# Kernel tuning notes

Measured on AMD Instinct MI355X. Metric: run time of the kernel, lower is better.

## Reference

```python
import jax, jax.numpy as jnp
import numpy as np

N_HEADS = 8
D_EMBED = 512
D_HEAD = D_EMBED // N_HEADS


def setup_inputs() -> dict:
    key = jax.random.key(0)
    ks = jax.random.split(key, 5)
    x = jax.random.normal(ks[0], (1, 4096, D_EMBED), dtype=jnp.float32)
    # in_proj: Linear(d, 3d); out_proj: Linear(d, d). Stored as [in, out] for x @ W.
    scale_in = 1.0 / np.sqrt(D_EMBED)
    W_in = jax.random.uniform(ks[1], (D_EMBED, 3 * D_EMBED), jnp.float32, -scale_in, scale_in)
    b_in = jax.random.uniform(ks[2], (3 * D_EMBED,), jnp.float32, -scale_in, scale_in)
    W_out = jax.random.uniform(ks[3], (D_EMBED, D_EMBED), jnp.float32, -scale_in, scale_in)
    b_out = jax.random.uniform(ks[4], (D_EMBED,), jnp.float32, -scale_in, scale_in)
    return {"x": x, "W_in": W_in, "b_in": b_in, "W_out": W_out, "b_out": b_out,
            "causal_mask": 1}


def reference(x, W_in, b_in, W_out, b_out, causal_mask):
    B, S, D = x.shape
    qkv = x @ W_in + b_in                      # [B, S, 3D]
    q, k, v = jnp.split(qkv, 3, axis=-1)
    # [B, S, D] -> [B, H, S, d_head]
    def split_heads(t):
        return t.reshape(B, S, N_HEADS, D_HEAD).transpose(0, 2, 1, 3)
    q, k, v = split_heads(q), split_heads(k), split_heads(v)
    weight = jnp.einsum("bhqd,bhkd->bhqk", q, k)  # [B, H, S, S]
    if causal_mask:
        mask = jnp.triu(jnp.ones((S, S), dtype=bool), k=1)
        weight = jnp.where(mask, -jnp.inf, weight)
    weight = weight / jnp.sqrt(jnp.float32(D_HEAD)).astype(weight.dtype)
    weight = jax.nn.softmax(weight, axis=-1)
    out = jnp.einsum("bhqk,bhkd->bhqd", weight, v)  # [B, H, S, d_head]
    out = out.transpose(0, 2, 1, 3).reshape(B, S, D)
    return out @ W_out + b_out
```

## Files before the change

kernel.cpp:

```cpp
#include <hip/hip_runtime.h>
#include <math.h>

#define SEQ 4096
#define DM 512
#define NH 8
#define DH 64
#define TQK (3 * DM)
#define QSCALE 0.18033688011112042f

typedef __attribute__((ext_vector_type(8))) short bf16x8;
typedef __attribute__((ext_vector_type(4))) float floatx4;
typedef unsigned short ushort_t;

__device__ __forceinline__ floatx4 mfma16(bf16x8 a, bf16x8 b, floatx4 c) {
    return __builtin_amdgcn_mfma_f32_16x16x32_bf16(a, b, c, 0, 0, 0);
}
__device__ __forceinline__ float ex2(float x) { return __builtin_amdgcn_exp2f(x); }

__device__ __forceinline__ unsigned int pk2(float a, float b) {
    unsigned int ua = __float_as_uint(a); ua = (ua + 0x7FFFu + ((ua >> 16) & 1u)) >> 16;
    unsigned int ub = __float_as_uint(b); ub = (ub + 0x7FFFu + ((ub >> 16) & 1u)) >> 16;
    return ua | (ub << 16);
}
__device__ __forceinline__ unsigned short f2bf(float x) {
    unsigned int u = __float_as_uint(x);
    return (unsigned short)((u + 0x7FFFu + ((u >> 16) & 1u)) >> 16);
}
__device__ __forceinline__ float bflo(unsigned int u) { return __uint_as_float(u << 16); }
__device__ __forceinline__ float bfhi(unsigned int u) { return __uint_as_float(u & 0xFFFF0000u); }

__device__ __forceinline__ void gload_lds16(const void* g, void* l) {
    __builtin_amdgcn_global_load_lds(
        (const __attribute__((address_space(1))) unsigned int*)g,
        (__attribute__((address_space(3))) unsigned int*)l, 16, 0, 0);
}

#define DPPMAX(x, ctrl) \
    (x) = fmaxf((x), __int_as_float(__builtin_amdgcn_update_dpp(0, __float_as_int(x), (ctrl), 0xF, 0xF, true)))
__device__ __forceinline__ float row_max16(float x) {
    DPPMAX(x, 0xB1);
    DPPMAX(x, 0x4E);
    DPPMAX(x, 0x141);
    DPPMAX(x, 0x140);
    return x;
}

__global__ __launch_bounds__(256) void prep(const float* __restrict__ x,
                                            const float* __restrict__ W_in,
                                            const float* __restrict__ W_out,
                                            ushort_t* __restrict__ xb,
                                            ushort_t* __restrict__ wti,
                                            ushort_t* __restrict__ wto) {
    __shared__ float T[64][65];
    const int bid = blockIdx.x, tid = threadIdx.x;
    if (bid < 1024) {
        const int i = bid * 256 + tid;
        const float4* p = (const float4*)x + (size_t)i * 2;
        float4 f0 = p[0], f1 = p[1];
        ((uint4*)xb)[i] = make_uint4(pk2(f0.x, f0.y), pk2(f0.z, f0.w),
                                     pk2(f1.x, f1.y), pk2(f1.z, f1.w));
        return;
    }
    const float* W; ushort_t* WT; int N, K, n0, k0; bool qscale;
    if (bid < 1216) { int id = bid - 1024; W = W_in;  WT = wti; N = TQK; K = DM;
                      n0 = (id % 24) * 64; k0 = (id / 24) * 64; qscale = true; }
    else            { int id = bid - 1216; W = W_out; WT = wto; N = DM;  K = DM;
                      n0 = (id % 8) * 64;  k0 = (id / 8) * 64;  qscale = false; }
    {
        const int r = tid >> 2, g = tid & 3;
        const float* src = W + (size_t)(k0 + r) * N + n0 + g * 16;
#pragma unroll
        for (int i = 0; i < 4; i++) {
            float4 f = ((const float4*)src)[i];
            T[g * 16 + i * 4 + 0][r] = f.x;
            T[g * 16 + i * 4 + 1][r] = f.y;
            T[g * 16 + i * 4 + 2][r] = f.z;
            T[g * 16 + i * 4 + 3][r] = f.w;
        }
    }
    __syncthreads();
    const int nr = tid >> 2, g2 = tid & 3;
    const float sc = (qscale && (n0 + nr < DM)) ? QSCALE : 1.0f;
    unsigned int pk[8];
#pragma unroll
    for (int j = 0; j < 8; j++)
        pk[j] = pk2(T[nr][g2 * 16 + 2 * j] * sc, T[nr][g2 * 16 + 2 * j + 1] * sc);
    ushort_t* dst = WT + (size_t)(n0 + nr) * K + k0 + g2 * 16;
    ((uint4*)dst)[0] = make_uint4(pk[0], pk[1], pk[2], pk[3]);
    ((uint4*)dst)[1] = make_uint4(pk[4], pk[5], pk[6], pk[7]);
}

template <bool OUT_BF16>
__global__ __launch_bounds__(256) void gemm128(const ushort_t* __restrict__ A,
                                               const ushort_t* __restrict__ BT,
                                               const float* __restrict__ bias,
                                               void* __restrict__ Cv,
                                               ushort_t* __restrict__ vt_out,
                                               int N, int K, int scale_q) {
    __shared__ __align__(16) ushort_t As[2][128 * 64];
    __shared__ __align__(16) ushort_t Bs[2][128 * 64];
    const int tid  = threadIdx.x;
    const int lane = tid & 63;
    const int w    = tid >> 6;
    const int quad = lane >> 4;
    const int ln   = lane & 15;
    const int row0 = blockIdx.y * 128;
    const int col0 = blockIdx.x * 128;
    const int wm = w >> 1, wn = w & 1;

    const int srow = lane >> 3;
    const int js   = (lane & 7) ^ srow;

    floatx4 acc[4][4];
#pragma unroll
    for (int i = 0; i < 4; i++)
#pragma unroll
        for (int j = 0; j < 4; j++) acc[i][j] = (floatx4){0.f, 0.f, 0.f, 0.f};

    const int nsteps = K >> 6;
#pragma unroll
    for (int i = 0; i < 4; i++) {
        const int c = w * 4 + i;
        gload_lds16(A  + (size_t)(row0 + c * 8 + srow) * K + js * 8, &As[0][c * 512]);
        gload_lds16(BT + (size_t)(col0 + c * 8 + srow) * K + js * 8, &Bs[0][c * 512]);
    }

    for (int kt = 0; kt < nsteps; kt++) {
        const int cur = kt & 1;
        __syncthreads();
        if (kt + 1 < nsteps) {
            const int k0n = (kt + 1) << 6;
#pragma unroll
            for (int i = 0; i < 4; i++) {
                const int c = w * 4 + i;
                gload_lds16(A  + (size_t)(row0 + c * 8 + srow) * K + k0n + js * 8, &As[cur ^ 1][c * 512]);
                gload_lds16(BT + (size_t)(col0 + c * 8 + srow) * K + k0n + js * 8, &Bs[cur ^ 1][c * 512]);
            }
        }
#pragma unroll
        for (int s = 0; s < 2; s++) {
            bf16x8 af[4], bfr[4];
#pragma unroll
            for (int i = 0; i < 4; i++) {
                const int lm = wm * 64 + i * 16 + ln;
                af[i] = *(const bf16x8*)&As[cur][lm * 64 + ((s * 4 + quad) ^ (ln & 7)) * 8];
                const int lnn = wn * 64 + i * 16 + ln;
                bfr[i] = *(const bf16x8*)&Bs[cur][lnn * 64 + ((s * 4 + quad) ^ (ln & 7)) * 8];
            }
#pragma unroll
            for (int i = 0; i < 4; i++)
#pragma unroll
                for (int j = 0; j < 4; j++)
                    acc[i][j] = mfma16(af[i], bfr[j], acc[i][j]);
        }
    }

    if (vt_out && col0 >= 2 * DM) {
#pragma unroll
        for (int j = 0; j < 4; j++) {
            const int n = col0 + wn * 64 + j * 16 + ln;
            const float bv = bias[n];
#pragma unroll
            for (int i = 0; i < 4; i++) {
                const int mb = row0 + wm * 64 + i * 16 + quad * 4;
                uint2 pkd;
                pkd.x = pk2(acc[i][j][0] + bv, acc[i][j][1] + bv);
                pkd.y = pk2(acc[i][j][2] + bv, acc[i][j][3] + bv);
                *(uint2*)&vt_out[(size_t)(n - 2 * DM) * SEQ + mb] = pkd;
            }
        }
        return;
    }

#pragma unroll
    for (int j = 0; j < 4; j++) {
        const int n = col0 + wn * 64 + j * 16 + ln;
        const float bv = bias[n] * ((scale_q && n < DM) ? QSCALE : 1.0f);
#pragma unroll
        for (int i = 0; i < 4; i++) {
            const int mb = row0 + wm * 64 + i * 16 + quad * 4;
#pragma unroll
            for (int r = 0; r < 4; r++) {
                const float v = acc[i][j][r] + bv;
                if (OUT_BF16) ((ushort_t*)Cv)[(size_t)(mb + r) * N + n] = f2bf(v);
                else          ((float*)Cv)[(size_t)(mb + r) * N + n] = v;
            }
        }
    }
}

__global__ __launch_bounds__(256) void attn_split(const ushort_t* __restrict__ qkv_b,
                                                  const ushort_t* __restrict__ vt,
                                                  ushort_t* __restrict__ po,
                                                  float2* __restrict__ pml) {
    __shared__ __align__(16) ushort_t Ks[2][64 * 64];
    __shared__ __align__(16) ushort_t Vs[2][64 * 64];
    __shared__ __align__(16) ushort_t Ps[64 * 72];

    const int tid  = threadIdx.x;
    const int lane = tid & 63;
    const int w    = tid >> 6;
    const int quad = lane >> 4;
    const int ln   = lane & 15;
    const int h    = blockIdx.y;

    const int e = 287 - (int)blockIdx.x;
    int k = 1;
    while (e >= 4 * k * (k + 1)) k++;
    const int off = e - 4 * k * (k - 1);
    const int qt  = 8 * (k - 1) + off / k;
    const int c   = off % k;
    const int nc  = k;
    const int T   = qt + 1;
    const int jt0 = (c * T) / nc;
    const int jt1 = ((c + 1) * T) / nc;
    const int q0  = qt * 64;

    const ushort_t* qrow = qkv_b + (size_t)(q0 + w * 16 + ln) * TQK + h * DH;
    const bf16x8 a0 = *(const bf16x8*)(qrow + quad * 8);
    const bf16x8 a1 = *(const bf16x8*)(qrow + quad * 8 + 32);

    const short oneb = (short)0x3F80;
    const bf16x8 vone = {oneb, oneb, oneb, oneb, oneb, oneb, oneb, oneb};

    float m_q = -INFINITY;
    floatx4 o[4], ol;
#pragma unroll
    for (int t = 0; t < 4; t++) o[t] = (floatx4){0.f, 0.f, 0.f, 0.f};
    ol = (floatx4){0.f, 0.f, 0.f, 0.f};

    const int srow = lane >> 3;
    const int js   = (lane & 7) ^ srow;

    {
        const int k0 = jt0 * 64;
#pragma unroll
        for (int i = 0; i < 2; i++) {
            const int cg = w * 2 + i;
            gload_lds16(qkv_b + (size_t)(k0 + cg * 8 + srow) * TQK + DM + h * DH + js * 8,
                        &Ks[0][cg * 512]);
            gload_lds16(vt + (size_t)(h * DH + cg * 8 + srow) * SEQ + k0 + js * 8,
                        &Vs[0][cg * 512]);
        }
    }

    for (int jt = jt0; jt < jt1; ++jt) {
        const int cur = (jt - jt0) & 1;
        __syncthreads();
        if (jt + 1 < jt1) {
            const int k0n = (jt + 1) * 64;
#pragma unroll
            for (int i = 0; i < 2; i++) {
                const int cg = w * 2 + i;
                gload_lds16(qkv_b + (size_t)(k0n + cg * 8 + srow) * TQK + DM + h * DH + js * 8,
                            &Ks[cur ^ 1][cg * 512]);
                gload_lds16(vt + (size_t)(h * DH + cg * 8 + srow) * SEQ + k0n + js * 8,
                            &Vs[cur ^ 1][cg * 512]);
            }
        }

        floatx4 sa[4];
#pragma unroll
        for (int t = 0; t < 4; t++) {
            const int n = t * 16 + ln;
            const bf16x8 b0 = *(const bf16x8*)&Ks[cur][n * 64 + ((quad) ^ (ln & 7)) * 8];
            const bf16x8 b1 = *(const bf16x8*)&Ks[cur][n * 64 + ((4 + quad) ^ (ln & 7)) * 8];
            floatx4 acc = {0.f, 0.f, 0.f, 0.f};
            acc = mfma16(a0, b0, acc);
            acc = mfma16(a1, b1, acc);
            sa[t] = acc;
        }

        if (jt == qt) {
#pragma unroll
            for (int t = 0; t < 4; t++) {
                const int cg2 = t * 16 + ln;
#pragma unroll
                for (int r = 0; r < 4; r++) {
                    const int rg = w * 16 + quad * 4 + r;
                    if (cg2 > rg) sa[t][r] = -INFINITY;
                }
            }
        }

        float mx = sa[0][0];
#pragma unroll
        for (int t = 0; t < 4; t++)
#pragma unroll
            for (int r = 0; r < 4; r++) mx = fmaxf(mx, sa[t][r]);
        mx = row_max16(mx);
        const float mn = fmaxf(m_q, mx);
        const float alpha = ex2(m_q - mn);
        m_q = mn;
#pragma unroll
        for (int t = 0; t < 4; t++)
#pragma unroll
            for (int r = 0; r < 4; r++) {
                const float p = ex2(sa[t][r] - mn);
                Ps[(w * 16 + quad * 4 + r) * 72 + t * 16 + ln] =
                    (ushort_t)(__float_as_uint(p) >> 16);
            }
        if (alpha < 1.0f) {
#pragma unroll
            for (int t = 0; t < 4; t++)
#pragma unroll
                for (int r = 0; r < 4; r++) o[t][r] *= alpha;
#pragma unroll
            for (int r = 0; r < 4; r++) ol[r] *= alpha;
        }

        __builtin_amdgcn_wave_barrier();

        const bf16x8 p0 = *(const bf16x8*)&Ps[(w * 16 + ln) * 72 + quad * 8];
        const bf16x8 p1 = *(const bf16x8*)&Ps[(w * 16 + ln) * 72 + quad * 8 + 32];
#pragma unroll
        for (int t = 0; t < 4; t++) {
            const int d = t * 16 + ln;
            const bf16x8 v0 = *(const bf16x8*)&Vs[cur][d * 64 + ((quad) ^ (ln & 7)) * 8];
            const bf16x8 v1 = *(const bf16x8*)&Vs[cur][d * 64 + ((4 + quad) ^ (ln & 7)) * 8];
            o[t] = mfma16(p0, v0, o[t]);
            o[t] = mfma16(p1, v1, o[t]);
        }
        ol = mfma16(p0, vone, ol);
        ol = mfma16(p1, vone, ol);
    }

    const size_t pbase  = ((size_t)h * 288 + e) * 4096;
    const size_t mlbase = ((size_t)h * 288 + e) * 64;
#pragma unroll
    for (int t = 0; t < 4; t++)
#pragma unroll
        for (int r = 0; r < 4; r++)
            po[pbase + (size_t)(w * 16 + quad * 4 + r) * 64 + t * 16 + ln] = f2bf(o[t][r]);
    if (ln == 0) {
#pragma unroll
        for (int r = 0; r < 4; r++)
            pml[mlbase + w * 16 + quad * 4 + r] = make_float2(m_q, ol[r]);
    }
}

__global__ __launch_bounds__(256) void attn_combine(const ushort_t* __restrict__ po,
                                                    const float2* __restrict__ pml,
                                                    ushort_t* __restrict__ aob) {
    const int qt = blockIdx.x, h = blockIdx.y;
    const int k = (qt >> 3) + 1;
    const int sbase = 4 * k * (k - 1) + (qt & 7) * k;
    const int nc = k;
    const int row = threadIdx.x >> 2, g = threadIdx.x & 3;

    float2 ml[8];
    float M = -INFINITY;
    for (int cidx = 0; cidx < nc; cidx++) {
        ml[cidx] = pml[((size_t)h * 288 + sbase + cidx) * 64 + row];
        M = fmaxf(M, ml[cidx].x);
    }
    float L = 0.f;
    float acc[16];
#pragma unroll
    for (int j = 0; j < 16; j++) acc[j] = 0.f;

    for (int cidx = 0; cidx < nc; cidx++) {
        const float wgt = ex2(ml[cidx].x - M);
        L += wgt * ml[cidx].y;
        const ushort_t* p = po + ((size_t)h * 288 + sbase + cidx) * 4096 + (size_t)row * 64 + g * 16;
        uint4 u0 = ((const uint4*)p)[0];
        uint4 u1 = ((const uint4*)p)[1];
        const unsigned int uu[8] = {u0.x, u0.y, u0.z, u0.w, u1.x, u1.y, u1.z, u1.w};
#pragma unroll
        for (int j = 0; j < 8; j++) {
            acc[2 * j]     += wgt * bflo(uu[j]);
            acc[2 * j + 1] += wgt * bfhi(uu[j]);
        }
    }
    const float inv = 1.0f / L;
    unsigned int pk[8];
#pragma unroll
    for (int j = 0; j < 8; j++)
        pk[j] = pk2(acc[2 * j] * inv, acc[2 * j + 1] * inv);
    ushort_t* dst = aob + (size_t)(qt * 64 + row) * DM + h * DH + g * 16;
    ((uint4*)dst)[0] = make_uint4(pk[0], pk[1], pk[2], pk[3]);
    ((uint4*)dst)[1] = make_uint4(pk[4], pk[5], pk[6], pk[7]);
}

extern "C" void kernel_launch(void* const* d_in, const int* in_sizes, int n_in,
                              void* d_out, int out_size, void* d_ws, size_t ws_size,
                              hipStream_t stream) {
    const float* x     = (const float*)d_in[0];
    const float* W_in  = (const float*)d_in[1];
    const float* b_in  = (const float*)d_in[2];
    const float* W_out = (const float*)d_in[3];
    const float* b_out = (const float*)d_in[4];
    float* out = (float*)d_out;

    char* ws = (char*)d_ws;
    ushort_t* xb    = (ushort_t*)ws;
    ushort_t* wti   = (ushort_t*)(ws + (4u  << 20));
    ushort_t* wto   = (ushort_t*)(ws + (6u  << 20));
    ushort_t* qkv_b = (ushort_t*)(ws + (7u  << 20));
    ushort_t* vtb   = (ushort_t*)(ws + (19u << 20));
    ushort_t* aob   = (ushort_t*)(ws + (23u << 20));
    ushort_t* po    = (ushort_t*)(ws + (27u << 20));
    float2*   pml   = (float2*)  (ws + (46u << 20));

    prep<<<1280, 256, 0, stream>>>(x, W_in, W_out, xb, wti, wto);

    gemm128<true><<<dim3(TQK / 128, SEQ / 128), 256, 0, stream>>>(
        xb, wti, b_in, qkv_b, vtb, TQK, DM, 1);

    attn_split<<<dim3(288, NH), 256, 0, stream>>>(qkv_b, vtb, po, pml);

    attn_combine<<<dim3(SEQ / 64, NH), 256, 0, stream>>>(po, pml, aob);

    gemm128<false><<<dim3(DM / 128, SEQ / 128), 256, 0, stream>>>(
        aob, wto, b_out, out, nullptr, DM, DM, 0);
}
```

Before: 173.7 us.

## Fuse split-KV combine into output GEMM and widen attention tiles to 128 queries

The attention split kernel now handles 128 query rows per block with 8 waves, halving the number of split work items and sharing each K/V tile load across twice as many queries. Causal masking becomes per-wave, with a clamp on the running max so fully masked rows stay finite. The separate combine kernel is removed: the output projection GEMM merges the partial results for each head directly into its LDS A tile, which drops the intermediate attention-output buffer and one launch. In exchange, each output-GEMM block redoes the combine for its rows once per column tile, and its global loads sit in the K-loop.

Result: no change. 173.4 us (-0.2%).

```diff
diff --git a/kernel.cpp b/kernel.cpp
--- a/kernel.cpp
+++ b/kernel.cpp
@@ -90,13 +90,11 @@
     ((uint4*)dst)[1] = make_uint4(pk[4], pk[5], pk[6], pk[7]);
 }
 
-template <bool OUT_BF16>
-__global__ __launch_bounds__(256) void gemm128(const ushort_t* __restrict__ A,
+__global__ __launch_bounds__(256) void gemm_in(const ushort_t* __restrict__ A,
                                                const ushort_t* __restrict__ BT,
                                                const float* __restrict__ bias,
-                                               void* __restrict__ Cv,
-                                               ushort_t* __restrict__ vt_out,
-                                               int N, int K, int scale_q) {
+                                               ushort_t* __restrict__ Cv,
+                                               ushort_t* __restrict__ vt_out) {
     __shared__ __align__(16) ushort_t As[2][128 * 64];
     __shared__ __align__(16) ushort_t Bs[2][128 * 64];
     const int tid  = threadIdx.x;
@@ -107,9 +105,9 @@
     const int row0 = blockIdx.y * 128;
     const int col0 = blockIdx.x * 128;
     const int wm = w >> 1, wn = w & 1;
-
     const int srow = lane >> 3;
     const int js   = (lane & 7) ^ srow;
+    const int K = DM, N = TQK;
 
     floatx4 acc[4][4];
 #pragma unroll
@@ -117,7 +115,6 @@
 #pragma unroll
         for (int j = 0; j < 4; j++) acc[i][j] = (floatx4){0.f, 0.f, 0.f, 0.f};
 
-    const int nsteps = K >> 6;
 #pragma unroll
     for (int i = 0; i < 4; i++) {
         const int c = w * 4 + i;
@@ -125,10 +122,10 @@
         gload_lds16(BT + (size_t)(col0 + c * 8 + srow) * K + js * 8, &Bs[0][c * 512]);
     }
 
-    for (int kt = 0; kt < nsteps; kt++) {
+    for (int kt = 0; kt < 8; kt++) {
         const int cur = kt & 1;
         __syncthreads();
-        if (kt + 1 < nsteps) {
+        if (kt < 7) {
             const int k0n = (kt + 1) << 6;
 #pragma unroll
             for (int i = 0; i < 4; i++) {
@@ -155,7 +152,7 @@
         }
     }
 
-    if (vt_out && col0 >= 2 * DM) {
+    if (col0 >= 2 * DM) {
 #pragma unroll
         for (int j = 0; j < 4; j++) {
             const int n = col0 + wn * 64 + j * 16 + ln;
@@ -175,27 +172,24 @@
 #pragma unroll
     for (int j = 0; j < 4; j++) {
         const int n = col0 + wn * 64 + j * 16 + ln;
-        const float bv = bias[n] * ((scale_q && n < DM) ? QSCALE : 1.0f);
+        const float bv = bias[n] * ((n < DM) ? QSCALE : 1.0f);
 #pragma unroll
         for (int i = 0; i < 4; i++) {
             const int mb = row0 + wm * 64 + i * 16 + quad * 4;
 #pragma unroll
-            for (int r = 0; r < 4; r++) {
-                const float v = acc[i][j][r] + bv;
-                if (OUT_BF16) ((ushort_t*)Cv)[(size_t)(mb + r) * N + n] = f2bf(v);
-                else          ((float*)Cv)[(size_t)(mb + r) * N + n] = v;
-            }
-        }
-    }
-}
-
-__global__ __launch_bounds__(256) void attn_split(const ushort_t* __restrict__ qkv_b,
+            for (int r = 0; r < 4; r++)
+                Cv[(size_t)(mb + r) * N + n] = f2bf(acc[i][j][r] + bv);
+        }
+    }
+}
+
+__global__ __launch_bounds__(512) void attn_split(const ushort_t* __restrict__ qkv_b,
                                                   const ushort_t* __restrict__ vt,
                                                   ushort_t* __restrict__ po,
                                                   float2* __restrict__ pml) {
     __shared__ __align__(16) ushort_t Ks[2][64 * 64];
     __shared__ __align__(16) ushort_t Vs[2][64 * 64];
-    __shared__ __align__(16) ushort_t Ps[64 * 72];
+    __shared__ __align__(16) ushort_t Ps[128 * 72];
 
     const int tid  = threadIdx.x;
     const int lane = tid & 63;
@@ -204,17 +198,17 @@
     const int ln   = lane & 15;
     const int h    = blockIdx.y;
 
-    const int e = 287 - (int)blockIdx.x;
-    int k = 1;
-    while (e >= 4 * k * (k + 1)) k++;
-    const int off = e - 4 * k * (k - 1);
-    const int qt  = 8 * (k - 1) + off / k;
-    const int c   = off % k;
-    const int nc  = k;
-    const int T   = qt + 1;
+    const int e = 143 - (int)blockIdx.x;
+    int g = 0;
+    while (e >= 2 * (g + 1) * (g + 2)) g++;
+    const int off = e - 2 * g * (g + 1);
+    const int nc  = g + 1;
+    const int qt  = 4 * g + off / nc;
+    const int c   = off % nc;
+    const int T   = 2 * qt + 2;
     const int jt0 = (c * T) / nc;
     const int jt1 = ((c + 1) * T) / nc;
-    const int q0  = qt * 64;
+    const int q0  = qt * 128;
 
     const ushort_t* qrow = qkv_b + (size_t)(q0 + w * 16 + ln) * TQK + h * DH;
     const bf16x8 a0 = *(const bf16x8*)(qrow + quad * 8);
@@ -234,29 +228,22 @@
 
     {
         const int k0 = jt0 * 64;
-#pragma unroll
-        for (int i = 0; i < 2; i++) {
-            const int cg = w * 2 + i;
-            gload_lds16(qkv_b + (size_t)(k0 + cg * 8 + srow) * TQK + DM + h * DH + js * 8,
-                        &Ks[0][cg * 512]);
-            gload_lds16(vt + (size_t)(h * DH + cg * 8 + srow) * SEQ + k0 + js * 8,
-                        &Vs[0][cg * 512]);
-        }
+        gload_lds16(qkv_b + (size_t)(k0 + w * 8 + srow) * TQK + DM + h * DH + js * 8,
+                    &Ks[0][w * 512]);
+        gload_lds16(vt + (size_t)(h * DH + w * 8 + srow) * SEQ + k0 + js * 8,
+                    &Vs[0][w * 512]);
     }
 
     for (int jt = jt0; jt < jt1; ++jt) {
         const int cur = (jt - jt0) & 1;
+        const int k0  = jt * 64;
         __syncthreads();
         if (jt + 1 < jt1) {
             const int k0n = (jt + 1) * 64;
-#pragma unroll
-            for (int i = 0; i < 2; i++) {
-                const int cg = w * 2 + i;
-                gload_lds16(qkv_b + (size_t)(k0n + cg * 8 + srow) * TQK + DM + h * DH + js * 8,
-                            &Ks[cur ^ 1][cg * 512]);
-                gload_lds16(vt + (size_t)(h * DH + cg * 8 + srow) * SEQ + k0n + js * 8,
-                            &Vs[cur ^ 1][cg * 512]);
-            }
+            gload_lds16(qkv_b + (size_t)(k0n + w * 8 + srow) * TQK + DM + h * DH + js * 8,
+                        &Ks[cur ^ 1][w * 512]);
+            gload_lds16(vt + (size_t)(h * DH + w * 8 + srow) * SEQ + k0n + js * 8,
+                        &Vs[cur ^ 1][w * 512]);
         }
 
         floatx4 sa[4];
@@ -271,13 +258,13 @@
             sa[t] = acc;
         }
 
-        if (jt == qt) {
+        if (k0 + 63 > q0 + w * 16) {
 #pragma unroll
             for (int t = 0; t < 4; t++) {
-                const int cg2 = t * 16 + ln;
+                const int cg2 = k0 + t * 16 + ln;
 #pragma unroll
                 for (int r = 0; r < 4; r++) {
-                    const int rg = w * 16 + quad * 4 + r;
+                    const int rg = q0 + w * 16 + quad * 4 + r;
                     if (cg2 > rg) sa[t][r] = -INFINITY;
                 }
             }
@@ -289,7 +276,7 @@
 #pragma unroll
             for (int r = 0; r < 4; r++) mx = fmaxf(mx, sa[t][r]);
         mx = row_max16(mx);
-        const float mn = fmaxf(m_q, mx);
+        const float mn = fmaxf(fmaxf(m_q, mx), -1e30f);
         const float alpha = ex2(m_q - mn);
         m_q = mn;
 #pragma unroll
@@ -325,8 +312,8 @@
         ol = mfma16(p1, vone, ol);
     }
 
-    const size_t pbase  = ((size_t)h * 288 + e) * 4096;
-    const size_t mlbase = ((size_t)h * 288 + e) * 64;
+    const size_t pbase  = ((size_t)h * 144 + e) * (128 * 64);
+    const size_t mlbase = ((size_t)h * 144 + e) * 128;
 #pragma unroll
     for (int t = 0; t < 4; t++)
 #pragma unroll
@@ -339,47 +326,123 @@
     }
 }
 
-__global__ __launch_bounds__(256) void attn_combine(const ushort_t* __restrict__ po,
-                                                    const float2* __restrict__ pml,
-                                                    ushort_t* __restrict__ aob) {
-    const int qt = blockIdx.x, h = blockIdx.y;
-    const int k = (qt >> 3) + 1;
-    const int sbase = 4 * k * (k - 1) + (qt & 7) * k;
-    const int nc = k;
-    const int row = threadIdx.x >> 2, g = threadIdx.x & 3;
-
-    float2 ml[8];
-    float M = -INFINITY;
-    for (int cidx = 0; cidx < nc; cidx++) {
-        ml[cidx] = pml[((size_t)h * 288 + sbase + cidx) * 64 + row];
-        M = fmaxf(M, ml[cidx].x);
-    }
-    float L = 0.f;
-    float acc[16];
-#pragma unroll
-    for (int j = 0; j < 16; j++) acc[j] = 0.f;
-
-    for (int cidx = 0; cidx < nc; cidx++) {
-        const float wgt = ex2(ml[cidx].x - M);
-        L += wgt * ml[cidx].y;
-        const ushort_t* p = po + ((size_t)h * 288 + sbase + cidx) * 4096 + (size_t)row * 64 + g * 16;
-        uint4 u0 = ((const uint4*)p)[0];
-        uint4 u1 = ((const uint4*)p)[1];
-        const unsigned int uu[8] = {u0.x, u0.y, u0.z, u0.w, u1.x, u1.y, u1.z, u1.w};
-#pragma unroll
-        for (int j = 0; j < 8; j++) {
-            acc[2 * j]     += wgt * bflo(uu[j]);
-            acc[2 * j + 1] += wgt * bfhi(uu[j]);
-        }
-    }
-    const float inv = 1.0f / L;
-    unsigned int pk[8];
-#pragma unroll
-    for (int j = 0; j < 8; j++)
-        pk[j] = pk2(acc[2 * j] * inv, acc[2 * j + 1] * inv);
-    ushort_t* dst = aob + (size_t)(qt * 64 + row) * DM + h * DH + g * 16;
-    ((uint4*)dst)[0] = make_uint4(pk[0], pk[1], pk[2], pk[3]);
-    ((uint4*)dst)[1] = make_uint4(pk[4], pk[5], pk[6], pk[7]);
+__global__ __launch_bounds__(512) void gemm_out(const ushort_t* __restrict__ po,
+                                                const float2* __restrict__ pml,
+                                                const ushort_t* __restrict__ BT,
+                                                const float* __restrict__ bias,
+                                                float* __restrict__ out) {
+    __shared__ __align__(16) ushort_t As[2][128 * 72];
+    __shared__ __align__(16) ushort_t Bs[2][128 * 64];
+    const int tid  = threadIdx.x;
+    const int lane = tid & 63;
+    const int w    = tid >> 6;
+    const int quad = lane >> 4;
+    const int ln   = lane & 15;
+    const int row0 = blockIdx.y * 128;
+    const int col0 = blockIdx.x * 128;
+    const int wm = w >> 2, wn = w & 3;
+    const int srow = lane >> 3;
+    const int js   = (lane & 7) ^ srow;
+
+    const int qt = blockIdx.y;
+    const int gq = qt >> 2;
+    const int nc = gq + 1;
+    const int sbase = 2 * gq * (gq + 1) + (qt & 3) * nc;
+
+    const int cr = tid >> 2, cg = tid & 3;
+
+    floatx4 acc[4][2];
+#pragma unroll
+    for (int i = 0; i < 4; i++)
+#pragma unroll
+        for (int j = 0; j < 2; j++) acc[i][j] = (floatx4){0.f, 0.f, 0.f, 0.f};
+
+    auto combine = [&](int head, int buf) {
+        float2 ml[8];
+        float M = -INFINITY;
+        for (int ci = 0; ci < nc; ci++) {
+            ml[ci] = pml[((size_t)head * 144 + sbase + ci) * 128 + cr];
+            M = fmaxf(M, ml[ci].x);
+        }
+        float L = 0.f;
+        float a[16];
+#pragma unroll
+        for (int j = 0; j < 16; j++) a[j] = 0.f;
+        for (int ci = 0; ci < nc; ci++) {
+            const float wgt = ex2(ml[ci].x - M);
+            L += wgt * ml[ci].y;
+            const ushort_t* p = po + ((size_t)head * 144 + sbase + ci) * (128 * 64)
+                                   + (size_t)cr * 64 + cg * 16;
+            uint4 u0 = ((const uint4*)p)[0];
+            uint4 u1 = ((const uint4*)p)[1];
+            const unsigned int uu[8] = {u0.x, u0.y, u0.z, u0.w, u1.x, u1.y, u1.z, u1.w};
+#pragma unroll
+            for (int j = 0; j < 8; j++) {
+                a[2 * j]     += wgt * bflo(uu[j]);
+                a[2 * j + 1] += wgt * bfhi(uu[j]);
+            }
+        }
+        const float inv = 1.0f / L;
+        unsigned int pk[8];
+#pragma unroll
+        for (int j = 0; j < 8; j++)
+            pk[j] = pk2(a[2 * j] * inv, a[2 * j + 1] * inv);
+        uint4* dst = (uint4*)&As[buf][cr * 72 + cg * 16];
+        dst[0] = make_uint4(pk[0], pk[1], pk[2], pk[3]);
+        dst[1] = make_uint4(pk[4], pk[5], pk[6], pk[7]);
+    };
+    auto loadB = [&](int kt, int buf) {
+#pragma unroll
+        for (int i = 0; i < 2; i++) {
+            const int cgrp = w * 2 + i;
+            gload_lds16(BT + (size_t)(col0 + cgrp * 8 + srow) * DM + kt * 64 + js * 8,
+                        &Bs[buf][cgrp * 512]);
+        }
+    };
+
+    loadB(0, 0);
+    combine(0, 0);
+
+    for (int kt = 0; kt < 8; kt++) {
+        const int cur = kt & 1;
+        __syncthreads();
+        if (kt < 7) {
+            loadB(kt + 1, cur ^ 1);
+            combine(kt + 1, cur ^ 1);
+        }
+#pragma unroll
+        for (int s = 0; s < 2; s++) {
+            bf16x8 af[4], bfr[2];
+#pragma unroll
+            for (int i = 0; i < 4; i++) {
+                const int lm = wm * 64 + i * 16 + ln;
+                af[i] = *(const bf16x8*)&As[cur][lm * 72 + (s * 4 + quad) * 8];
+            }
+#pragma unroll
+            for (int j = 0; j < 2; j++) {
+                const int lnn = wn * 32 + j * 16 + ln;
+                bfr[j] = *(const bf16x8*)&Bs[cur][lnn * 64 + ((s * 4 + quad) ^ (ln & 7)) * 8];
+            }
+#pragma unroll
+            for (int i = 0; i < 4; i++)
+#pragma unroll
+                for (int j = 0; j < 2; j++)
+                    acc[i][j] = mfma16(af[i], bfr[j], acc[i][j]);
+        }
+    }
+
+#pragma unroll
+    for (int j = 0; j < 2; j++) {
+        const int n = col0 + wn * 32 + j * 16 + ln;
+        const float bv = bias[n];
+#pragma unroll
+        for (int i = 0; i < 4; i++) {
+            const int mb = row0 + wm * 64 + i * 16 + quad * 4;
+#pragma unroll
+            for (int r = 0; r < 4; r++)
+                out[(size_t)(mb + r) * DM + n] = acc[i][j][r] + bv;
+        }
+    }
 }
 
 extern "C" void kernel_launch(void* const* d_in, const int* in_sizes, int n_in,
@@ -398,19 +461,14 @@
     ushort_t* wto   = (ushort_t*)(ws + (6u  << 20));
     ushort_t* qkv_b = (ushort_t*)(ws + (7u  << 20));
     ushort_t* vtb   = (ushort_t*)(ws + (19u << 20));
-    ushort_t* aob   = (ushort_t*)(ws + (23u << 20));
-    ushort_t* po    = (ushort_t*)(ws + (27u << 20));
-    float2*   pml   = (float2*)  (ws + (46u << 20));
+    ushort_t* po    = (ushort_t*)(ws + (23u << 20));
+    float2*   pml   = (float2*)  (ws + (42u << 20));
 
     prep<<<1280, 256, 0, stream>>>(x, W_in, W_out, xb, wti, wto);
 
-    gemm128<true><<<dim3(TQK / 128, SEQ / 128), 256, 0, stream>>>(
-        xb, wti, b_in, qkv_b, vtb, TQK, DM, 1);
-
-    attn_split<<<dim3(288, NH), 256, 0, stream>>>(qkv_b, vtb, po, pml);
-
-    attn_combine<<<dim3(SEQ / 64, NH), 256, 0, stream>>>(po, pml, aob);
-
-    gemm128<false><<<dim3(DM / 128, SEQ / 128), 256, 0, stream>>>(
-        aob, wto, b_out, out, nullptr, DM, DM, 0);
-}
+    gemm_in<<<dim3(TQK / 128, SEQ / 128), 256, 0, stream>>>(xb, wti, b_in, qkv_b, vtb);
+
+    attn_split<<<dim3(144, NH), 512, 0, stream>>>(qkv_b, vtb, po, pml);
+
+    gemm_out<<<dim3(DM / 128, SEQ / 128), 512, 0, stream>>>(po, pml, wto, b_out, out);
+}
```
